# Optimization experiments

Hardware: AMD Instinct MI355X
Metric: run time of the kernel (lower is better)

Reference implementation:

```python
import jax, jax.numpy as jnp
import numpy as np

B, C1, C2, H, W = 8, 256, 256, 64, 64
C = 256            # int(c1*e)
G = C // 16        # 16 groups (dg)
Cg = C // G        # 16 channels per group
K = 9              # 3x3 kernel sample points
BN_EPS = 1e-5

# kernel grid offsets for 3x3, dilation 1 (pad=1 centers the grid)
KH = jnp.array([-1, -1, -1, 0, 0, 0, 1, 1, 1], jnp.float32)
KW = jnp.array([-1, 0, 1, -1, 0, 1, -1, 0, 1], jnp.float32)


def setup_inputs() -> dict:
    key = jax.random.key(0)
    ks = jax.random.split(key, 10)
    x = jax.random.normal(ks[0], (B, C1, H, W), jnp.float32)
    w_cv1 = jax.random.normal(ks[1], (C, C1), jnp.float32) / np.sqrt(C1)
    b_cv1 = jax.random.normal(ks[2], (C,), jnp.float32) * 0.1
    # offset/mask linear (DCNv4 inits to zero; small scale keeps sampling sane)
    w_off = jax.random.normal(ks[3], (G * 3 * K, C), jnp.float32) * 0.01
    b_off = jax.random.normal(ks[4], (G * 3 * K,), jnp.float32) * 0.01
    w_cv2 = jax.random.normal(ks[5], (C2, C), jnp.float32) / np.sqrt(C)
    bn_gamma = jax.random.uniform(ks[6], (C2,), jnp.float32, 0.5, 1.5)
    bn_beta = jax.random.normal(ks[7], (C2,), jnp.float32) * 0.1
    bn_mean = jax.random.normal(ks[8], (C2,), jnp.float32) * 0.1
    bn_var = jax.random.uniform(ks[9], (C2,), jnp.float32, 0.5, 1.5)
    return dict(x=x, w_cv1=w_cv1, b_cv1=b_cv1, w_off=w_off, b_off=b_off,
                w_cv2=w_cv2, bn_gamma=bn_gamma, bn_beta=bn_beta,
                bn_mean=bn_mean, bn_var=bn_var)


def _gather(vflat, hi, wi):
    # vflat: (B, H*W, G, Cg); hi/wi: (B,H,W,K,G) float corner indices
    ok = ((hi >= 0) & (hi < H) & (wi >= 0) & (wi < W)).astype(vflat.dtype)
    idx = (jnp.clip(hi, 0, H - 1) * W + jnp.clip(wi, 0, W - 1)).astype(jnp.int32)
    idx = idx.reshape(B, H * W * K, G)
    idxb = jnp.broadcast_to(idx[..., None], (B, H * W * K, G, Cg))
    g = jnp.take_along_axis(vflat, idxb, axis=1)  # (B, HWK, G, Cg)
    return g.reshape(B, H, W, K, G, Cg), ok


def _dcnv4(v, off, mask):
    # v: (B,H,W,G,Cg); off: (B,H,W,G,K,2) (dh,dw); mask: (B,H,W,G,K)
    ii = jnp.arange(H, dtype=jnp.float32)
    jj = jnp.arange(W, dtype=jnp.float32)
    ph = ii[None, :, None, None, None] + KH[None, None, None, None, :] + off[..., 0]
    pw = jj[None, None, :, None, None] + KW[None, None, None, None, :] + off[..., 1]
    ph = ph.transpose(0, 1, 2, 4, 3)  # (B,H,W,K,G)
    pw = pw.transpose(0, 1, 2, 4, 3)
    h0 = jnp.floor(ph); w0 = jnp.floor(pw)
    ah = ph - h0; aw = pw - w0
    vflat = v.reshape(B, H * W, G, Cg)
    g00, ok00 = _gather(vflat, h0, w0)
    g01, ok01 = _gather(vflat, h0, w0 + 1)
    g10, ok10 = _gather(vflat, h0 + 1, w0)
    g11, ok11 = _gather(vflat, h0 + 1, w0 + 1)
    w00 = ((1 - ah) * (1 - aw) * ok00)[..., None]
    w01 = ((1 - ah) * aw * ok01)[..., None]
    w10 = (ah * (1 - aw) * ok10)[..., None]
    w11 = (ah * aw * ok11)[..., None]
    sample = w00 * g00 + w01 * g01 + w10 * g10 + w11 * g11  # (B,H,W,K,G,Cg)
    out = jnp.einsum('bhwkgc,bhwgk->bhwgc', sample, mask)
    return out.reshape(B, H, W, C).transpose(0, 3, 1, 2)  # NCHW


def reference(x, w_cv1, b_cv1, w_off, b_off, w_cv2, bn_gamma, bn_beta, bn_mean, bn_var):
    # cv1: 1x1 conv
    h1 = jnp.einsum('bchw,oc->bohw', x, w_cv1) + b_cv1[None, :, None, None]
    # offset/mask 1x1 projection, per-group layout [2K offsets, K masks]
    om = jnp.einsum('bchw,oc->bhwo', h1, w_off) + b_off
    om = om.reshape(B, H, W, G, 3 * K)
    off = om[..., :2 * K].reshape(B, H, W, G, K, 2)
    mask = om[..., 2 * K:]  # DCNv4: no softmax, used directly
    v = h1.transpose(0, 2, 3, 1).reshape(B, H, W, G, Cg)
    y = _dcnv4(v, off, mask)
    # cv2: 1x1 conv (no bias)
    y = jnp.einsum('bchw,oc->bohw', y, w_cv2)
    # BatchNorm (eval mode)
    scale = (bn_gamma / jnp.sqrt(bn_var + BN_EPS))[None, :, None, None]
    y = (y - bn_mean[None, :, None, None]) * scale + bn_beta[None, :, None, None]
    # SiLU
    return y * jax.nn.sigmoid(y)
```

## Files before the change

### kernel.cpp

```cpp
#include <hip/hip_runtime.h>

#define HW 4096
#define CCH 256
#define MOFF 432
#define PTOT 32768
#define PDIM 68
#define PIMG (PDIM*PDIM)

typedef unsigned short u16;
typedef __attribute__((ext_vector_type(8))) short short8;
typedef __attribute__((ext_vector_type(8))) unsigned short u16x8;
typedef __attribute__((ext_vector_type(4))) unsigned short u16x4;
typedef __attribute__((ext_vector_type(4))) float f32x4;

__device__ __forceinline__ u16 f2b(float f){
  unsigned int u = __float_as_uint(f);
  unsigned int rounding = 0x7FFFu + ((u >> 16) & 1u);
  return (u16)((u + rounding) >> 16);
}
__device__ __forceinline__ float b2f(u16 s){
  return __uint_as_float(((unsigned int)s) << 16);
}

__global__ __launch_bounds__(256) void k_cvtw(const float* __restrict__ w1,
    const float* __restrict__ woff, const float* __restrict__ w2,
    const float* __restrict__ gamma, const float* __restrict__ beta,
    const float* __restrict__ mean, const float* __restrict__ var,
    u16* __restrict__ wb1, u16* __restrict__ wboff, u16* __restrict__ wb2,
    float* __restrict__ bnA, float* __restrict__ bnB, u16* __restrict__ h1p){
  int r = blockIdx.x, t = threadIdx.x;
  if (r < 256) wb1[r*256 + t] = f2b(w1[r*256 + t]);
  else if (r < 704){ int o = r - 256; wboff[o*256 + t] = (o < MOFF) ? f2b(woff[o*256 + t]) : (u16)0; }
  else if (r < 960){ int o = r - 704; wb2[o*256 + t] = f2b(w2[o*256 + t]); }
  else if (r == 960){
    if (t < 256){
      float sc = gamma[t] * rsqrtf(var[t] + 1e-5f);
      bnA[t] = sc;
      bnB[t] = beta[t] - mean[t] * sc;
    }
  } else {
    int n = (r - 961) * 8 + (t >> 5);
    int seg = t & 31;
    int img = n / 528, m = n % 528;
    int row, col;
    if (m < 136){ row = m / 68; col = m % 68; }
    else if (m < 272){ int mm = m - 136; row = 66 + mm / 68; col = mm % 68; }
    else { int mm = m - 272; row = 2 + (mm >> 2); int c4 = mm & 3; col = (c4 & 1) + 66 * (c4 >> 1); }
    u16x8 z = {};
    *reinterpret_cast<u16x8*>(&h1p[((size_t)img * PIMG + row * PDIM + col) * 256 + seg * 8]) = z;
  }
}

__global__ __launch_bounds__(256) void k_xt(const float* __restrict__ x,
    u16* __restrict__ xT){
  __shared__ float tile[64][65];
  const int pb = blockIdx.x * 64, cb = blockIdx.y * 64, b = blockIdx.z;
  const int t = threadIdx.x;
  const float* src = x + ((size_t)(b * CCH + cb)) * HW + pb;
  #pragma unroll
  for (int pass = 0; pass < 4; ++pass){
    int c_l = pass * 16 + (t >> 4);
    int pq = (t & 15) * 4;
    float4 v = *reinterpret_cast<const float4*>(&src[(size_t)c_l * HW + pq]);
    tile[pq + 0][c_l] = v.x; tile[pq + 1][c_l] = v.y;
    tile[pq + 2][c_l] = v.z; tile[pq + 3][c_l] = v.w;
  }
  __syncthreads();
  #pragma unroll
  for (int pass = 0; pass < 4; ++pass){
    int p_l = pass * 16 + (t >> 4);
    int cq = (t & 15) * 4;
    u16x4 o4;
    #pragma unroll
    for (int j = 0; j < 4; ++j) o4[j] = f2b(tile[p_l][cq + j]);
    *reinterpret_cast<u16x4*>(&xT[((size_t)b * HW + pb + p_l) * CCH + cb + cq]) = o4;
  }
}

template<int BN, bool GUARD, bool SILU, int AMODE, bool PADC>
__global__ __launch_bounds__(256) void k_gemm(const void* __restrict__ Asrc,
    const u16* __restrict__ Bw, const float* __restrict__ bias,
    const float* __restrict__ bnB, void* __restrict__ Cout, int ldc, int NL){
  constexpr int WN = BN / 2;
  constexpr int MF = 4;
  constexpr int NF = WN / 16;
  constexpr int BOFF = 128 * 40;
  constexpr int STG = (128 + BN) * 40;
  constexpr int CMAT = 128 * (BN + 8);
  constexpr int SM = SILU ? STG : (STG > CMAT ? STG : CMAT);
  __shared__ __align__(16) u16 smem[SM];

  const int t = threadIdx.x;
  const int tm = blockIdx.x * 128;
  const int tn = blockIdx.y * BN;
  const int lane = t & 63;
  const int wid = t >> 6;
  const int wr = wid >> 1, wc = wid & 1;

  f32x4 acc[MF][NF] = {};

  for (int kc = 0; kc < 256; kc += 32){
    if constexpr (AMODE == 2){
      const u16* Ap = (const u16*)Asrc;
      #pragma unroll
      for (int i = 0; i < 2; ++i){
        int v = t + i * 256;
        int row = v >> 2, cq = v & 3;
        int p = tm + row;
        int bb = p >> 12, ii = (p >> 6) & 63, jj = p & 63;
        size_t base = ((size_t)(bb * PIMG) + (ii + 2) * PDIM + jj + 2) * 256;
        *reinterpret_cast<u16x8*>(&smem[row * 40 + cq * 8]) =
          *reinterpret_cast<const u16x8*>(&Ap[base + kc + cq * 8]);
      }
    } else {
      const u16* Ap = (const u16*)Asrc;
      #pragma unroll
      for (int i = 0; i < 2; ++i){
        int v = t + i * 256;
        int row = v >> 2, cq = v & 3;
        *reinterpret_cast<u16x8*>(&smem[row * 40 + cq * 8]) =
          *reinterpret_cast<const u16x8*>(&Ap[(size_t)(tm + row) * 256 + kc + cq * 8]);
      }
    }
    constexpr int BV = BN * 4 / 256;
    #pragma unroll
    for (int i = 0; i < BV; ++i){
      int v = t + i * 256;
      int row = v >> 2, cq = v & 3;
      *reinterpret_cast<u16x8*>(&smem[BOFF + row * 40 + cq * 8]) =
        *reinterpret_cast<const u16x8*>(&Bw[(size_t)(tn + row) * 256 + kc + cq * 8]);
    }
    __syncthreads();
    short8 af[MF], bf[NF];
    #pragma unroll
    for (int m = 0; m < MF; ++m)
      af[m] = *reinterpret_cast<const short8*>(
        &smem[(wr * 64 + m * 16 + (lane & 15)) * 40 + (lane >> 4) * 8]);
    #pragma unroll
    for (int n = 0; n < NF; ++n)
      bf[n] = *reinterpret_cast<const short8*>(
        &smem[BOFF + (wc * WN + n * 16 + (lane & 15)) * 40 + (lane >> 4) * 8]);
    #pragma unroll
    for (int m = 0; m < MF; ++m)
      #pragma unroll
      for (int n = 0; n < NF; ++n)
        acc[m][n] = __builtin_amdgcn_mfma_f32_16x16x32_bf16(af[m], bf[n], acc[m][n], 0, 0, 0);
    __syncthreads();
  }

  if constexpr (SILU){
    const int bimg = tm >> 12;
    const int ploc = tm & 4095;
    float* outp = (float*)Cout;
    #pragma unroll
    for (int n = 0; n < NF; ++n){
      int o = tn + wc * WN + n * 16 + (lane & 15);
      float sA = bias[o], sB = bnB[o];
      #pragma unroll
      for (int m = 0; m < MF; ++m){
        int prow = wr * 64 + m * 16 + ((lane >> 4) << 2);
        f32x4 st;
        #pragma unroll
        for (int j = 0; j < 4; ++j){
          float y = acc[m][n][j] * sA + sB;
          st[j] = y / (1.f + expf(-y));
        }
        *reinterpret_cast<f32x4*>(&outp[((size_t)(bimg * 256 + o)) * HW + ploc + prow]) = st;
      }
    }
  } else {
    constexpr int CP = BN + 8;
    u16* C_l = smem;
    #pragma unroll
    for (int n = 0; n < NF; ++n){
      int col = wc * WN + n * 16 + (lane & 15);
      int o = tn + col;
      float bi = (!GUARD || o < NL) ? bias[o] : 0.f;
      #pragma unroll
      for (int m = 0; m < MF; ++m){
        int r0 = wr * 64 + m * 16 + ((lane >> 4) << 2);
        #pragma unroll
        for (int j = 0; j < 4; ++j)
          C_l[(r0 + j) * CP + col] = f2b(acc[m][n][j] + bi);
      }
    }
    __syncthreads();
    constexpr int SEG = BN / 8;
    constexpr int RPP = 256 / SEG;
    u16* Co = (u16*)Cout;
    #pragma unroll
    for (int pass = 0; pass < 128 / RPP; ++pass){
      int row = pass * RPP + t / SEG;
      int sg = t % SEG;
      int oc = tn + sg * 8;
      if constexpr (PADC){
        int p = tm + row;
        int bb = p >> 12, ii = (p >> 6) & 63, jj = p & 63;
        size_t dst = ((size_t)(bb * PIMG) + (ii + 2) * PDIM + jj + 2) * 256 + oc;
        *reinterpret_cast<u16x8*>(&Co[dst]) =
          *reinterpret_cast<const u16x8*>(&C_l[row * CP + sg * 8]);
      } else {
        if (!GUARD || oc + 8 <= NL)
          *reinterpret_cast<u16x8*>(&Co[(size_t)(tm + row) * ldc + oc]) =
            *reinterpret_cast<const u16x8*>(&C_l[row * CP + sg * 8]);
      }
    }
  }
}

__global__ __launch_bounds__(256) void k_sample(const u16* __restrict__ h1p,
    const u16* __restrict__ om, u16* __restrict__ ydcn){
  __shared__ float oms[8 * MOFF];
  const int t = threadIdx.x;
  const int pblk = blockIdx.x * 8;
  {
    const u16* src = om + (size_t)pblk * MOFF;
    #pragma unroll
    for (int i = 0; i < 2; ++i){
      int idx = t + i * 256;
      if (idx < 432){
        u16x8 v = *reinterpret_cast<const u16x8*>(&src[idx * 8]);
        float4 lo, hi;
        lo.x = b2f(v[0]); lo.y = b2f(v[1]); lo.z = b2f(v[2]); lo.w = b2f(v[3]);
        hi.x = b2f(v[4]); hi.y = b2f(v[5]); hi.z = b2f(v[6]); hi.w = b2f(v[7]);
        *reinterpret_cast<float4*>(&oms[idx * 8]) = lo;
        *reinterpret_cast<float4*>(&oms[idx * 8 + 4]) = hi;
      }
    }
  }
  __syncthreads();

  const int pix = t >> 5, s = t & 31;
  const int g = s >> 1, half = s & 1;
  const int p = pblk + pix;
  const int b = p >> 12, hw = p & 4095;
  const int ic = hw >> 6, jc = hw & 63;
  const u16* vb = h1p + (size_t)b * PIMG * 256 + g * 16 + half * 8;
  const float* ob = &oms[pix * MOFF + g * 27];
  const float fi = (float)ic, fj = (float)jc;

  float acc[8] = {};
  #pragma unroll
  for (int k = 0; k < 9; ++k){
    float oh = ob[2 * k], ow = ob[2 * k + 1], m = ob[18 + k];
    float ph = fi + (float)(k / 3 - 1) + oh;
    float pw = fj + (float)(k % 3 - 1) + ow;
    float h0f = floorf(ph), w0f = floorf(pw);
    float ah = ph - h0f, aw = pw - w0f;
    int h0 = (int)h0f, w0 = (int)w0f;
    int hc = min(max(h0, -2), 64) + 2;
    int wc = min(max(w0, -2), 64) + 2;
    const u16* c0 = &vb[(hc * PDIM + wc) * 256];
    const u16* c1 = c0 + PDIM * 256;
    float mh1 = m * ah, mh0 = m - mh1;
    float c01w = mh0 * aw, c00w = mh0 - c01w;
    float c11w = mh1 * aw, c10w = mh1 - c11w;
    u16x8 a00 = *reinterpret_cast<const u16x8*>(c0);
    u16x8 a01 = *reinterpret_cast<const u16x8*>(c0 + 256);
    u16x8 a10 = *reinterpret_cast<const u16x8*>(c1);
    u16x8 a11 = *reinterpret_cast<const u16x8*>(c1 + 256);
    #pragma unroll
    for (int j = 0; j < 8; ++j){
      acc[j] += c00w * b2f(a00[j]) + c01w * b2f(a01[j])
              + c10w * b2f(a10[j]) + c11w * b2f(a11[j]);
    }
  }
  u16x8 o8;
  #pragma unroll
  for (int j = 0; j < 8; ++j) o8[j] = f2b(acc[j]);
  *reinterpret_cast<u16x8*>(&ydcn[(size_t)p * 256 + g * 16 + half * 8]) = o8;
}

extern "C" void kernel_launch(void* const* d_in, const int* in_sizes, int n_in,
                              void* d_out, int out_size, void* d_ws, size_t ws_size,
                              hipStream_t stream) {
  const float* x     = (const float*)d_in[0];
  const float* w1    = (const float*)d_in[1];
  const float* b1    = (const float*)d_in[2];
  const float* woff  = (const float*)d_in[3];
  const float* boff  = (const float*)d_in[4];
  const float* w2    = (const float*)d_in[5];
  const float* gamma = (const float*)d_in[6];
  const float* beta  = (const float*)d_in[7];
  const float* mean  = (const float*)d_in[8];
  const float* var   = (const float*)d_in[9];
  float* out = (float*)d_out;
  (void)in_sizes; (void)n_in; (void)out_size; (void)ws_size;

  u16* h1p   = (u16*)d_ws;
  u16* om    = h1p + (size_t)8 * PIMG * 256;
  u16* xT    = om + (size_t)PTOT * MOFF;
  u16* ydcn  = xT;
  u16* wb1   = xT + (size_t)PTOT * CCH;
  u16* wboff = wb1 + 256 * 256;
  u16* wb2   = wboff + 448 * 256;
  float* bnA = (float*)(wb2 + 256 * 256);
  float* bnB = bnA + 256;

  dim3 blk(256);
  k_cvtw<<<dim3(1489), blk, 0, stream>>>(w1, woff, w2, gamma, beta, mean, var,
                                         wb1, wboff, wb2, bnA, bnB, h1p);
  k_xt<<<dim3(64, 4, 8), blk, 0, stream>>>(x, xT);
  k_gemm<128, false, false, 0, true><<<dim3(PTOT / 128, 2), blk, 0, stream>>>(
      (const void*)xT, wb1, b1, nullptr, (void*)h1p, 0, 256);
  k_gemm<64, true, false, 2, false><<<dim3(PTOT / 128, 7), blk, 0, stream>>>(
      (const void*)h1p, wboff, boff, nullptr, (void*)om, MOFF, MOFF);
  k_sample<<<dim3(PTOT / 8), blk, 0, stream>>>(h1p, om, ydcn);
  k_gemm<128, false, true, 0, false><<<dim3(PTOT / 128, 2), blk, 0, stream>>>(
      (const void*)ydcn, wb2, bnA, bnB, (void*)out, 0, 256);
}
```

Baseline: 109.2 us.

## Store padded h1 as per-group planes and gather bilinear corners contiguously

Changes the padded h1 buffer from pixel-major (256 channels per pixel) to group-planar layout (16 channels per pixel per group plane). The writers (cv1 GEMM epilogue, border zeroing) and the reader (offset GEMM) are updated to match. The sampling kernel now uses 4 threads per group, 4 pixels per block. Each thread loads one 16-byte corner chunk from the top row and one from the bottom row, and the left/right halves are combined with a shuffle. This makes the two horizontal corners of a row one contiguous 64-byte read, improving gather coalescing. In exchange it doubles the sample-kernel thread count, adds a shuffle reduction, and makes the GEMM A-loads and stores strided across planes.

```diff
diff --git a/kernel.cpp b/kernel.cpp
--- a/kernel.cpp
+++ b/kernel.cpp
@@ -39,15 +39,15 @@
       bnB[t] = beta[t] - mean[t] * sc;
     }
   } else {
-    int n = (r - 961) * 8 + (t >> 5);
-    int seg = t & 31;
-    int img = n / 528, m = n % 528;
+    int n = (r - 961) * 128 + (t >> 1);
+    int seg = t & 1;
+    int plane = n / 528, m = n % 528;
     int row, col;
     if (m < 136){ row = m / 68; col = m % 68; }
     else if (m < 272){ int mm = m - 136; row = 66 + mm / 68; col = mm % 68; }
     else { int mm = m - 272; row = 2 + (mm >> 2); int c4 = mm & 3; col = (c4 & 1) + 66 * (c4 >> 1); }
     u16x8 z = {};
-    *reinterpret_cast<u16x8*>(&h1p[((size_t)img * PIMG + row * PDIM + col) * 256 + seg * 8]) = z;
+    *reinterpret_cast<u16x8*>(&h1p[((size_t)plane * PIMG + row * PDIM + col) * 16 + seg * 8]) = z;
   }
 }
 
@@ -108,9 +108,10 @@
         int row = v >> 2, cq = v & 3;
         int p = tm + row;
         int bb = p >> 12, ii = (p >> 6) & 63, jj = p & 63;
-        size_t base = ((size_t)(bb * PIMG) + (ii + 2) * PDIM + jj + 2) * 256;
+        int c = kc + cq * 8;
+        size_t base = ((size_t)(bb * 16 + (c >> 4)) * PIMG + (ii + 2) * PDIM + jj + 2) * 16 + (c & 15);
         *reinterpret_cast<u16x8*>(&smem[row * 40 + cq * 8]) =
-          *reinterpret_cast<const u16x8*>(&Ap[base + kc + cq * 8]);
+          *reinterpret_cast<const u16x8*>(&Ap[base]);
       }
     } else {
       const u16* Ap = (const u16*)Asrc;
@@ -196,7 +197,7 @@
       if constexpr (PADC){
         int p = tm + row;
         int bb = p >> 12, ii = (p >> 6) & 63, jj = p & 63;
-        size_t dst = ((size_t)(bb * PIMG) + (ii + 2) * PDIM + jj + 2) * 256 + oc;
+        size_t dst = ((size_t)(bb * 16 + (oc >> 4)) * PIMG + (ii + 2) * PDIM + jj + 2) * 16 + (oc & 15);
         *reinterpret_cast<u16x8*>(&Co[dst]) =
           *reinterpret_cast<const u16x8*>(&C_l[row * CP + sg * 8]);
       } else {
@@ -210,34 +211,29 @@
 
 __global__ __launch_bounds__(256) void k_sample(const u16* __restrict__ h1p,
     const u16* __restrict__ om, u16* __restrict__ ydcn){
-  __shared__ float oms[8 * MOFF];
+  __shared__ float oms[4 * MOFF];
   const int t = threadIdx.x;
-  const int pblk = blockIdx.x * 8;
-  {
-    const u16* src = om + (size_t)pblk * MOFF;
-    #pragma unroll
-    for (int i = 0; i < 2; ++i){
-      int idx = t + i * 256;
-      if (idx < 432){
-        u16x8 v = *reinterpret_cast<const u16x8*>(&src[idx * 8]);
-        float4 lo, hi;
-        lo.x = b2f(v[0]); lo.y = b2f(v[1]); lo.z = b2f(v[2]); lo.w = b2f(v[3]);
-        hi.x = b2f(v[4]); hi.y = b2f(v[5]); hi.z = b2f(v[6]); hi.w = b2f(v[7]);
-        *reinterpret_cast<float4*>(&oms[idx * 8]) = lo;
-        *reinterpret_cast<float4*>(&oms[idx * 8 + 4]) = hi;
-      }
-    }
+  const int pblk = blockIdx.x * 4;
+  if (t < 216){
+    u16x8 v = *reinterpret_cast<const u16x8*>(&om[(size_t)pblk * MOFF + t * 8]);
+    float4 lo, hi;
+    lo.x = b2f(v[0]); lo.y = b2f(v[1]); lo.z = b2f(v[2]); lo.w = b2f(v[3]);
+    hi.x = b2f(v[4]); hi.y = b2f(v[5]); hi.z = b2f(v[6]); hi.w = b2f(v[7]);
+    *reinterpret_cast<float4*>(&oms[t * 8]) = lo;
+    *reinterpret_cast<float4*>(&oms[t * 8 + 4]) = hi;
   }
   __syncthreads();
 
-  const int pix = t >> 5, s = t & 31;
-  const int g = s >> 1, half = s & 1;
-  const int p = pblk + pix;
+  const int px = t >> 6;
+  const int g = (t >> 2) & 15;
+  const int q = t & 3;
+  const int p = pblk + px;
   const int b = p >> 12, hw = p & 4095;
   const int ic = hw >> 6, jc = hw & 63;
-  const u16* vb = h1p + (size_t)b * PIMG * 256 + g * 16 + half * 8;
-  const float* ob = &oms[pix * MOFF + g * 27];
+  const u16* plane = h1p + (size_t)(b * 16 + g) * PIMG * 16;
+  const float* ob = &oms[px * MOFF + g * 27];
   const float fi = (float)ic, fj = (float)jc;
+  const bool wsel = (q >= 2);
 
   float acc[8] = {};
   #pragma unroll
@@ -250,25 +246,25 @@
     int h0 = (int)h0f, w0 = (int)w0f;
     int hc = min(max(h0, -2), 64) + 2;
     int wc = min(max(w0, -2), 64) + 2;
-    const u16* c0 = &vb[(hc * PDIM + wc) * 256];
-    const u16* c1 = c0 + PDIM * 256;
+    const u16* cbase = plane + ((hc * PDIM + wc) << 4) + (q << 3);
+    u16x8 tv = *reinterpret_cast<const u16x8*>(cbase);
+    u16x8 bv = *reinterpret_cast<const u16x8*>(cbase + PDIM * 16);
     float mh1 = m * ah, mh0 = m - mh1;
-    float c01w = mh0 * aw, c00w = mh0 - c01w;
-    float c11w = mh1 * aw, c10w = mh1 - c11w;
-    u16x8 a00 = *reinterpret_cast<const u16x8*>(c0);
-    u16x8 a01 = *reinterpret_cast<const u16x8*>(c0 + 256);
-    u16x8 a10 = *reinterpret_cast<const u16x8*>(c1);
-    u16x8 a11 = *reinterpret_cast<const u16x8*>(c1 + 256);
-    #pragma unroll
-    for (int j = 0; j < 8; ++j){
-      acc[j] += c00w * b2f(a00[j]) + c01w * b2f(a01[j])
-              + c10w * b2f(a10[j]) + c11w * b2f(a11[j]);
-    }
-  }
-  u16x8 o8;
+    float awq = wsel ? aw : (1.f - aw);
+    float ct = mh0 * awq, cb = mh1 * awq;
+    #pragma unroll
+    for (int j = 0; j < 8; ++j)
+      acc[j] += ct * b2f(tv[j]) + cb * b2f(bv[j]);
+  }
   #pragma unroll
-  for (int j = 0; j < 8; ++j) o8[j] = f2b(acc[j]);
-  *reinterpret_cast<u16x8*>(&ydcn[(size_t)p * 256 + g * 16 + half * 8]) = o8;
+  for (int j = 0; j < 8; ++j)
+    acc[j] += __shfl_xor(acc[j], 2, 64);
+  if (q < 2){
+    u16x8 o8;
+    #pragma unroll
+    for (int j = 0; j < 8; ++j) o8[j] = f2b(acc[j]);
+    *reinterpret_cast<u16x8*>(&ydcn[(size_t)p * 256 + g * 16 + q * 8]) = o8;
+  }
 }
 
 extern "C" void kernel_launch(void* const* d_in, const int* in_sizes, int n_in,
@@ -288,7 +284,7 @@
   (void)in_sizes; (void)n_in; (void)out_size; (void)ws_size;
 
   u16* h1p   = (u16*)d_ws;
-  u16* om    = h1p + (size_t)8 * PIMG * 256;
+  u16* om    = h1p + (size_t)128 * PIMG * 16;
   u16* xT    = om + (size_t)PTOT * MOFF;
   u16* ydcn  = xT;
   u16* wb1   = xT + (size_t)PTOT * CCH;
@@ -305,7 +301,7 @@
       (const void*)xT, wb1, b1, nullptr, (void*)h1p, 0, 256);
   k_gemm<64, true, false, 2, false><<<dim3(PTOT / 128, 7), blk, 0, stream>>>(
       (const void*)h1p, wboff, boff, nullptr, (void*)om, MOFF, MOFF);
-  k_sample<<<dim3(PTOT / 8), blk, 0, stream>>>(h1p, om, ydcn);
+  k_sample<<<dim3(PTOT / 4), blk, 0, stream>>>(h1p, om, ydcn);
   k_gemm<128, false, true, 0, false><<<dim3(PTOT / 128, 2), blk, 0, stream>>>(
       (const void*)ydcn, wb2, bnA, bnB, (void*)out, 0, 256);
 }
```

Measured after the change: 105.0 us. 1.04x faster.
